# Optimization experiments

Measured on AMD Instinct MI355X. Metric: run time of the kernel, lower is better.

The kernel has to match this reference:

```python
import jax, jax.numpy as jnp
import numpy as np

NUM_HEADS = 8
NUM_KV_HEADS = 4
HEAD_DIM = 256
HIDDEN = 2048
SEQ = 4096
CHUNK_START = 2048
CHUNK_END = 4096
SOFTCAP = 50.0
EPS = 1e-6
ROPE_THETA = 10000.0
NEG_INF = -1e9


def _rms_norm(x, w, eps=EPS):
    # Gemma RMSNorm: computed in fp32, scale is (1 + w)
    x32 = x.astype(jnp.float32)
    out = x32 * jax.lax.rsqrt(jnp.mean(x32 * x32, axis=-1, keepdims=True) + eps)
    return (out * (1.0 + w.astype(jnp.float32))).astype(x.dtype)


def _rotate_half(x):
    h = x.shape[-1] // 2
    return jnp.concatenate([-x[..., h:], x[..., :h]], axis=-1)


def _apply_rope(x, cos, sin):
    # x: [B, S, H, D]; cos/sin: [B, S, D] -> unsqueeze head dim
    cos = cos[:, :, None, :]
    sin = sin[:, :, None, :]
    return x * cos + _rotate_half(x) * sin


def setup_inputs() -> dict:
    key = jax.random.key(0)
    ks = jax.random.split(key, 8)
    hidden_states = jax.random.normal(ks[0], (1, SEQ, HIDDEN), dtype=jnp.float32)
    # real RoPE tables
    inv_freq = 1.0 / (ROPE_THETA ** (np.arange(0, HEAD_DIM, 2, dtype=np.float32) / HEAD_DIM))
    pos = np.arange(SEQ, dtype=np.float32)
    freqs = np.outer(pos, inv_freq)                      # [S, D/2]
    emb = np.concatenate([freqs, freqs], axis=-1)        # [S, D]
    cos = jnp.asarray(np.cos(emb))[None]                 # [1, S, D]
    sin = jnp.asarray(np.sin(emb))[None]
    # causal additive mask for the chunk: query i (abs pos start+i) attends keys j <= start+i
    q_pos = np.arange(CHUNK_START, CHUNK_END)[:, None]
    k_pos = np.arange(CHUNK_END)[None, :]
    attention_mask = jnp.asarray(np.where(k_pos <= q_pos, 0.0, NEG_INF).astype(np.float32))[None, None]
    s = 0.02
    wq = jax.random.normal(ks[1], (HIDDEN, NUM_HEADS * HEAD_DIM), dtype=jnp.float32) * s
    wk = jax.random.normal(ks[2], (HIDDEN, NUM_KV_HEADS * HEAD_DIM), dtype=jnp.float32) * s
    wv = jax.random.normal(ks[3], (HIDDEN, NUM_KV_HEADS * HEAD_DIM), dtype=jnp.float32) * s
    wo = jax.random.normal(ks[4], (NUM_HEADS * HEAD_DIM, HIDDEN), dtype=jnp.float32) * s
    q_norm_w = jnp.zeros((HEAD_DIM,), dtype=jnp.float32)
    k_norm_w = jnp.zeros((HEAD_DIM,), dtype=jnp.float32)
    v_norm_w = jnp.zeros((HEAD_DIM,), dtype=jnp.float32)
    return {
        'hidden_states': hidden_states, 'cos': cos, 'sin': sin,
        'attention_mask': attention_mask,
        'wq': wq, 'wk': wk, 'wv': wv, 'wo': wo,
        'q_norm_w': q_norm_w, 'k_norm_w': k_norm_w, 'v_norm_w': v_norm_w,
        'start': CHUNK_START, 'end': CHUNK_END,
    }


def reference(hidden_states, cos, sin, attention_mask, wq, wk, wv, wo,
              q_norm_w, k_norm_w, v_norm_w, start, end):
    B = hidden_states.shape[0]
    chunk = end - start
    scaling = HEAD_DIM ** -0.5

    # ---- queries from the chunk ----
    q = (hidden_states[:, start:end] @ wq).reshape(B, chunk, NUM_HEADS, HEAD_DIM)
    q = _rms_norm(q, q_norm_w)
    q = _apply_rope(q, cos[:, start:end], sin[:, start:end])
    q = q.transpose(0, 2, 1, 3)                         # [B, H, chunk, D]

    # ---- keys / values over [0, end) ----
    kv_h = hidden_states[:, :end]
    k = (kv_h @ wk).reshape(B, end, NUM_KV_HEADS, HEAD_DIM)
    k = _rms_norm(k, k_norm_w)
    k = _apply_rope(k, cos[:, :end], sin[:, :end]).transpose(0, 2, 1, 3)   # [B, KV, end, D]
    v = (kv_h @ wv).reshape(B, end, NUM_KV_HEADS, HEAD_DIM)
    v = _rms_norm(v, v_norm_w).transpose(0, 2, 1, 3)                        # [B, KV, end, D]

    # ---- GQA repeat_kv ----
    n_rep = NUM_HEADS // NUM_KV_HEADS
    k = jnp.repeat(k, n_rep, axis=1)                    # [B, H, end, D]
    v = jnp.repeat(v, n_rep, axis=1)

    # ---- eager attention with logit softcap ----
    logits = jnp.einsum('bhqd,bhkd->bhqk', q, k) * scaling
    logits = jnp.tanh(logits / SOFTCAP) * SOFTCAP
    logits = logits + attention_mask
    attn = jax.nn.softmax(logits.astype(jnp.float32), axis=-1).astype(q.dtype)
    out = jnp.einsum('bhqk,bhkd->bhqd', attn, v)
    out = out.transpose(0, 2, 1, 3).reshape(B, chunk, NUM_HEADS * HEAD_DIM)
    return out @ wo
```

## Files before the change

kernel.cpp:

```cpp
#include <hip/hip_runtime.h>

#define HID 2048
#define SEQL 4096
#define CHUNK 2048
#define NHEADS 8
#define NKVH 4
#define HDIM 256

typedef __bf16 bf16x4 __attribute__((ext_vector_type(4)));
typedef __bf16 bf16x8 __attribute__((ext_vector_type(8)));
typedef float f32x4 __attribute__((ext_vector_type(4)));
typedef _Float16 f16x4 __attribute__((ext_vector_type(4)));
typedef __attribute__((address_space(1))) unsigned int* as1_u32;
typedef __attribute__((address_space(3))) unsigned int* as3_u32;

__device__ __forceinline__ void load_lds16(const __bf16* g, __bf16* l) {
  __builtin_amdgcn_global_load_lds((as1_u32)g, (as3_u32)l, 16, 0, 0);
}

__global__ void cvt_bf16_kernel(const float* __restrict__ X, __bf16* __restrict__ Y) {
  int i = blockIdx.x * blockDim.x + threadIdx.x;
  const float4* xv = (const float4*)X;
  float4 v = xv[i];
  bf16x4 o;
  o[0] = (__bf16)v.x; o[1] = (__bf16)v.y; o[2] = (__bf16)v.z; o[3] = (__bf16)v.w;
  *(bf16x4*)(Y + i * 4) = o;
}

__global__ void transpose_all_kernel(const float* __restrict__ wq, const float* __restrict__ wk,
                                     const float* __restrict__ wv, const float* __restrict__ wo,
                                     __bf16* __restrict__ WQT, __bf16* __restrict__ WKVT,
                                     __bf16* __restrict__ WOT) {
  __shared__ float tile[64][65];
  const int b = blockIdx.x;
  const float* W;
  __bf16* WT;
  int R, C, bx, by;
  if (b < 1024) { W = wq; WT = WQT; R = 2048; C = 2048; bx = b & 31; by = b >> 5; }
  else if (b < 1536) { int q = b - 1024; W = wk; WT = WKVT; R = 2048; C = 1024; bx = q & 15; by = q >> 4; }
  else if (b < 2048) { int q = b - 1536; W = wv; WT = WKVT + (size_t)1024 * 2048; R = 2048; C = 1024; bx = q & 15; by = q >> 4; }
  else { int q = b - 2048; W = wo; WT = WOT; R = 2048; C = 2048; bx = q & 31; by = q >> 5; }
  int r0 = by * 64, c0 = bx * 64;
  for (int i = threadIdx.x; i < 4096; i += 256) {
    int r = i >> 6, c = i & 63;
    tile[r][c] = W[(size_t)(r0 + r) * C + c0 + c];
  }
  __syncthreads();
  for (int i = threadIdx.x; i < 4096; i += 256) {
    int c = i >> 6, r = i & 63;
    WT[(size_t)(c0 + c) * R + r0 + r] = (__bf16)tile[r][c];
  }
}

template <int MODE>
__global__ __launch_bounds__(512, 2) void gemm256_kernel(
    const __bf16* __restrict__ A0, const __bf16* __restrict__ B0,
    const __bf16* __restrict__ B1, void* __restrict__ C0, void* __restrict__ C1) {
  __shared__ __bf16 Asm[2][256 * 64];
  __shared__ __bf16 Bsm[2][256 * 64];
  const int tid = threadIdx.x;
  const int lane = tid & 63, wave = tid >> 6;
  const int quad = lane >> 4, l15 = lane & 15;
  const int wm = (wave & 1) * 128, wn = (wave >> 1) * 64;

  const __bf16 *A, *B;
  char* Cb;
  int m0, n0;
  if (MODE == 0) {
    int b = blockIdx.x;
    if (b < 128) { A = A0; B = B0; Cb = (char*)C0; m0 = (b & 15) * 256; n0 = (b >> 4) * 256; }
    else { int q = b - 128; A = A0 + (size_t)2048 * 2048; B = B1; Cb = (char*)C1; m0 = (q & 7) * 256; n0 = (q >> 3) * 256; }
  } else {
    A = A0; B = B0; Cb = (char*)C0;
    m0 = (int)(blockIdx.x & 7) * 256; n0 = (int)(blockIdx.x >> 3) * 256;
  }

  f32x4 acc[8][4];
#pragma unroll
  for (int i = 0; i < 8; i++)
#pragma unroll
    for (int j = 0; j < 4; j++) acc[i][j] = (f32x4){0.f, 0.f, 0.f, 0.f};

  const int rr = tid >> 3;
  const int gch = (tid & 7) ^ ((tid >> 3) & 7);
  const int ldsb = wave * 512;

  const int sx = l15 & 7;
  const int s0 = ((0 + quad) ^ sx) * 8;
  const int s1 = ((4 + quad) ^ sx) * 8;

#define STAGE(T, BF)                                                                  \
  {                                                                                   \
    const int k0s = (T) * 64;                                                         \
    _Pragma("unroll")                                                                 \
    for (int a = 0; a < 4; a++) {                                                     \
      load_lds16(A + (size_t)(m0 + a * 64 + rr) * 2048 + k0s + gch * 8,               \
                 &Asm[BF][a * 4096 + ldsb]);                                          \
      load_lds16(B + (size_t)(n0 + a * 64 + rr) * 2048 + k0s + gch * 8,               \
                 &Bsm[BF][a * 4096 + ldsb]);                                          \
    }                                                                                 \
  }

#define LDA(MH, BF)                                                                   \
  _Pragma("unroll")                                                                   \
  for (int mi = 0; mi < 4; mi++) {                                                    \
    const int rowb = (wm + (MH) * 64 + mi * 16 + l15) * 64;                           \
    af[mi * 2 + 0] = *(const bf16x8*)(&Asm[BF][rowb + s0]);                           \
    af[mi * 2 + 1] = *(const bf16x8*)(&Asm[BF][rowb + s1]);                           \
  }

#define LDB(DST, NH, BF)                                                              \
  _Pragma("unroll")                                                                   \
  for (int ni = 0; ni < 2; ni++) {                                                    \
    const int rowb = (wn + (NH) * 32 + ni * 16 + l15) * 64;                           \
    DST[ni * 2 + 0] = *(const bf16x8*)(&Bsm[BF][rowb + s0]);                          \
    DST[ni * 2 + 1] = *(const bf16x8*)(&Bsm[BF][rowb + s1]);                          \
  }

#define MMA(MH, NH, BV)                                                               \
  __builtin_amdgcn_s_setprio(1);                                                      \
  _Pragma("unroll")                                                                   \
  for (int mi = 0; mi < 4; mi++)                                                      \
    _Pragma("unroll")                                                                 \
    for (int ni = 0; ni < 2; ni++) {                                                  \
      acc[(MH) * 4 + mi][(NH) * 2 + ni] = __builtin_amdgcn_mfma_f32_16x16x32_bf16(    \
          af[mi * 2 + 0], BV[ni * 2 + 0], acc[(MH) * 4 + mi][(NH) * 2 + ni], 0, 0, 0);\
      acc[(MH) * 4 + mi][(NH) * 2 + ni] = __builtin_amdgcn_mfma_f32_16x16x32_bf16(    \
          af[mi * 2 + 1], BV[ni * 2 + 1], acc[(MH) * 4 + mi][(NH) * 2 + ni], 0, 0, 0);\
    }                                                                                 \
  __builtin_amdgcn_s_setprio(0);

  bf16x8 af[8], bX[4], bY[4];

  STAGE(0, 0);
  STAGE(1, 1);
  asm volatile("s_waitcnt vmcnt(8)" ::: "memory");
  __builtin_amdgcn_s_barrier();

  const int NT = 32;
#pragma unroll 2
  for (int t = 0; t < NT; t++) {
    const int c = t & 1;
    LDA(0, c); LDB(bX, 0, c);
    __builtin_amdgcn_s_barrier();
    MMA(0, 0, bX);
    __builtin_amdgcn_s_barrier();
    LDB(bY, 1, c);
    __builtin_amdgcn_s_barrier();
    MMA(0, 1, bY);
    __builtin_amdgcn_s_barrier();
    LDA(1, c);
    __builtin_amdgcn_s_barrier();
    MMA(1, 1, bY);
    __builtin_amdgcn_s_barrier();
    LDB(bX, 0, c);
    __builtin_amdgcn_s_barrier();
    MMA(1, 0, bX);
    __builtin_amdgcn_s_barrier();
    if (t + 2 < NT) {
      STAGE(t + 2, c);
      asm volatile("s_waitcnt vmcnt(8)" ::: "memory");
      __builtin_amdgcn_s_barrier();
    } else if (t + 1 < NT) {
      asm volatile("s_waitcnt vmcnt(0)" ::: "memory");
      __builtin_amdgcn_s_barrier();
    }
  }

#pragma unroll
  for (int mh = 0; mh < 2; mh++)
#pragma unroll
    for (int mi = 0; mi < 4; mi++) {
      const int r = m0 + wm + mh * 64 + mi * 16 + quad * 4;
#pragma unroll
      for (int ni = 0; ni < 4; ni++) {
        const int cc = n0 + wn + (ni >> 1) * 32 + (ni & 1) * 16 + l15;
#pragma unroll
        for (int j = 0; j < 4; j++) {
          if (MODE == 1)
            ((float*)Cb)[(size_t)(r + j) * 2048 + cc] = acc[mh * 4 + mi][ni][j];
          else
            ((__bf16*)Cb)[(size_t)(r + j) * 2048 + cc] = (__bf16)acc[mh * 4 + mi][ni][j];
        }
      }
    }
#undef STAGE
#undef LDA
#undef LDB
#undef MMA
}

template <int NI, bool F32OUT>
__global__ __launch_bounds__(256, 2) void gemm_bt_kernel(
    const __bf16* __restrict__ A, const __bf16* __restrict__ B,
    void* __restrict__ Cv, int M, int N, int Kd) {
  constexpr int BN = NI * 32;
  __shared__ __bf16 Asm[2][128 * 32];
  __shared__ __bf16 Bsm[2][BN * 32];
  const int tid = threadIdx.x;
  const int lane = tid & 63, wave = tid >> 6;
  const int quad = lane >> 4, l15 = lane & 15;
  const int m0 = blockIdx.x * 128, n0 = blockIdx.y * BN;
  const int wm = (wave & 1) * 64, wn = (wave >> 1) * (NI * 16);
  f32x4 acc[4][NI];
#pragma unroll
  for (int i = 0; i < 4; i++)
#pragma unroll
    for (int j = 0; j < NI; j++) acc[i][j] = (f32x4){0.f, 0.f, 0.f, 0.f};

  const int rA = lane >> 2, cA = (lane & 3) * 8;

#pragma unroll
  for (int c = wave; c < 8; c += 4)
    load_lds16(A + (size_t)(m0 + c * 16 + rA) * Kd + cA, &Asm[0][c * 512]);
#pragma unroll
  for (int c = wave; c < BN / 16; c += 4)
    load_lds16(B + (size_t)(n0 + c * 16 + rA) * Kd + cA, &Bsm[0][c * 512]);

  for (int k0 = 0; k0 < Kd; k0 += 32) {
    const int buf = (k0 >> 5) & 1;
    __syncthreads();
    if (k0 + 32 < Kd) {
#pragma unroll
      for (int c = wave; c < 8; c += 4)
        load_lds16(A + (size_t)(m0 + c * 16 + rA) * Kd + k0 + 32 + cA, &Asm[buf ^ 1][c * 512]);
#pragma unroll
      for (int c = wave; c < BN / 16; c += 4)
        load_lds16(B + (size_t)(n0 + c * 16 + rA) * Kd + k0 + 32 + cA, &Bsm[buf ^ 1][c * 512]);
    }
    bf16x8 af[4], bfr[NI];
#pragma unroll
    for (int i = 0; i < 4; i++)
      af[i] = *(const bf16x8*)(&Asm[buf][(wm + i * 16 + l15) * 32 + quad * 8]);
#pragma unroll
    for (int i = 0; i < NI; i++)
      bfr[i] = *(const bf16x8*)(&Bsm[buf][(wn + i * 16 + l15) * 32 + quad * 8]);
#pragma unroll
    for (int mi = 0; mi < 4; mi++)
#pragma unroll
      for (int ni = 0; ni < NI; ni++)
        acc[mi][ni] = __builtin_amdgcn_mfma_f32_16x16x32_bf16(af[mi], bfr[ni], acc[mi][ni], 0, 0, 0);
  }
#pragma unroll
  for (int mi = 0; mi < 4; mi++) {
    int r = m0 + wm + mi * 16 + quad * 4;
#pragma unroll
    for (int ni = 0; ni < NI; ni++) {
      int cc = n0 + wn + ni * 16 + l15;
#pragma unroll
      for (int j = 0; j < 4; j++) {
        if (F32OUT)
          ((float*)Cv)[(size_t)(r + j) * N + cc] = acc[mi][ni][j];
        else
          ((__bf16*)Cv)[(size_t)(r + j) * N + cc] = (__bf16)acc[mi][ni][j];
      }
    }
  }
}

__global__ void norm_all_kernel(__bf16* __restrict__ Qp, __bf16* __restrict__ KVp,
                                const float* __restrict__ cosb, const float* __restrict__ sinb,
                                const float* __restrict__ qw, const float* __restrict__ kw,
                                const float* __restrict__ vw) {
  const int gw = (blockIdx.x * 256 + threadIdx.x) >> 6;
  const int lane = threadIdx.x & 63;
  const int d0 = lane * 4;

  __bf16* row;
  const float* w;
  int pos = -1;
  bool isV = false;
  float prescale = 1.f;
  if (gw < 16384) {
    int t = gw >> 3, h = gw & 7;
    row = Qp + (size_t)t * 2048 + h * 256;
    w = qw; pos = t + 2048; prescale = 0.0625f;
  } else {
    int g2 = gw - 16384;
    int t = g2 >> 3, r = g2 & 7;
    if (r < 4) {
      row = KVp + (size_t)t * 2048 + r * 256;
      w = kw; pos = t;
    } else {
      row = KVp + (size_t)t * 2048 + 1024 + (r - 4) * 256;
      w = vw; isV = true;
    }
  }

  bf16x4 rv = *(const bf16x4*)(row + d0);
  float x[4];
  float ss = 0.f;
#pragma unroll
  for (int j = 0; j < 4; j++) { x[j] = (float)rv[j]; ss += x[j] * x[j]; }
#pragma unroll
  for (int off = 1; off < 64; off <<= 1) ss += __shfl_xor(ss, off);
  float scale = rsqrtf(ss * (1.f / 256.f) + 1e-6f);
  float n[4];
#pragma unroll
  for (int j = 0; j < 4; j++) n[j] = x[j] * scale * (1.f + w[d0 + j]);

  if (!isV) {
    const float* cp = cosb + (size_t)pos * 256 + d0;
    const float* sp = sinb + (size_t)pos * 256 + d0;
    bf16x4 ov;
#pragma unroll
    for (int j = 0; j < 4; j++) {
      float other = __shfl_xor(n[j], 32);
      float rot = (lane < 32) ? -other : other;
      ov[j] = (__bf16)((n[j] * cp[j] + rot * sp[j]) * prescale);
    }
    *(bf16x4*)(row + d0) = ov;
  } else {
    bf16x4 ov;
#pragma unroll
    for (int j = 0; j < 4; j++) ov[j] = (__bf16)n[j];
    *(bf16x4*)(row + d0) = ov;
  }
}

__global__ void vtrans_kernel(const __bf16* __restrict__ KVp, __bf16* __restrict__ VT) {
  __shared__ __bf16 tile[64][72];
  const int b = blockIdx.x;
  const int h = b >> 8;
  const int r = b & 255;
  const int t0 = (r >> 2) * 64;
  const int d0 = (r & 3) * 64;
  const __bf16* src = KVp + 1024 + h * 256 + d0;
#pragma unroll
  for (int it = 0; it < 2; it++) {
    int idx = it * 256 + threadIdx.x;
    int tt = idx >> 3, dd = (idx & 7) * 8;
    *(bf16x8*)(&tile[tt][dd]) = *(const bf16x8*)(src + (size_t)(t0 + tt) * 2048 + dd);
  }
  __syncthreads();
  __bf16* dst = VT + (size_t)h * (256 * 4096) + (size_t)d0 * 4096 + t0;
#pragma unroll
  for (int it = 0; it < 2; it++) {
    int idx = it * 256 + threadIdx.x;
    int dd = idx >> 3, tt = (idx & 7) * 8;
    bf16x8 o;
#pragma unroll
    for (int j = 0; j < 8; j++) o[j] = tile[tt + j][dd];
    *(bf16x8*)(dst + (size_t)dd * 4096 + tt) = o;
  }
}

__global__ __launch_bounds__(256, 2) void attn_kernel(
    const __bf16* __restrict__ Q,
    const __bf16* __restrict__ K,
    const __bf16* __restrict__ VT,
    _Float16* __restrict__ Op,
    float* __restrict__ Lp) {
  __shared__ __bf16 Ksm[2][8][32][32];
  __shared__ __bf16 Vsm[2][256][32];
  __shared__ __bf16 Pex[4][32][40];
  const int tid = threadIdx.x;
  const int lane = tid & 63, wave = tid >> 6;
  const int quad = lane >> 4, l15 = lane & 15;
  const int b = blockIdx.x;
  const int idx = b & 255;
  const int h = idx & 7, sp = (idx >> 3) & 3;
  int qt = idx >> 5;
  if (b >= 256) qt = 15 - qt;
  const int kvh = h >> 1;

  const int T = 68 + 4 * qt;
  const int nst = T >> 2;

  bf16x8 qf[2][8];
#pragma unroll
  for (int r = 0; r < 2; r++) {
    const __bf16* qp = Q + (size_t)(qt * 128 + wave * 32 + r * 16 + l15) * 2048 + h * 256 + quad * 8;
#pragma unroll
    for (int s = 0; s < 8; s++) qf[r][s] = *(const bf16x8*)(qp + s * 32);
  }
  f32x4 o[2][16];
#pragma unroll
  for (int r = 0; r < 2; r++)
#pragma unroll
    for (int i = 0; i < 16; i++) o[r][i] = (f32x4){0.f, 0.f, 0.f, 0.f};
  float rs[2][4] = {{0.f, 0.f, 0.f, 0.f}, {0.f, 0.f, 0.f, 0.f}};

  const __bf16* Kb = K + kvh * 256;
  const __bf16* Vb = VT + (size_t)kvh * (256 * 4096);
  const int rA = lane >> 2;
  const int cAs = (((lane & 3) ^ ((rA >> 1) & 3)) * 8);
  const int kx = (quad ^ ((l15 >> 1) & 3)) * 8;
  const int qbase = 2048 + qt * 128 + wave * 32 + quad * 4;

  {
    const int t0 = sp * 32;
#pragma unroll
    for (int ch = 0; ch < 4; ch++) {
      int cc = wave + ch * 4;
      int s = cc >> 1, hf = cc & 1;
      load_lds16(Kb + (size_t)(t0 + hf * 16 + rA) * 2048 + s * 32 + cAs, &Ksm[0][s][hf * 16][0]);
      load_lds16(Vb + (size_t)(cc * 16 + rA) * 4096 + t0 + cAs, &Vsm[0][cc * 16][0]);
    }
  }

  for (int i = 0; i < nst; i++) {
    const int buf = i & 1;
    const int t0 = (4 * i + sp) * 32;
    __syncthreads();
    if (i + 1 < nst) {
      const int t1 = t0 + 128;
#pragma unroll
      for (int ch = 0; ch < 4; ch++) {
        int cc = wave + ch * 4;
        int s = cc >> 1, hf = cc & 1;
        load_lds16(Kb + (size_t)(t1 + hf * 16 + rA) * 2048 + s * 32 + cAs, &Ksm[buf ^ 1][s][hf * 16][0]);
        load_lds16(Vb + (size_t)(cc * 16 + rA) * 4096 + t1 + cAs, &Vsm[buf ^ 1][cc * 16][0]);
      }
    }

    f32x4 s4[2][2];
    s4[0][0] = (f32x4){0.f, 0.f, 0.f, 0.f};
    s4[0][1] = s4[0][0]; s4[1][0] = s4[0][0]; s4[1][1] = s4[0][0];
#pragma unroll
    for (int s = 0; s < 8; s++) {
      bf16x8 b0 = *(const bf16x8*)(&Ksm[buf][s][l15][kx]);
      bf16x8 b1 = *(const bf16x8*)(&Ksm[buf][s][16 + l15][kx]);
      s4[0][0] = __builtin_amdgcn_mfma_f32_16x16x32_bf16(qf[0][s], b0, s4[0][0], 0, 0, 0);
      s4[0][1] = __builtin_amdgcn_mfma_f32_16x16x32_bf16(qf[0][s], b1, s4[0][1], 0, 0, 0);
      s4[1][0] = __builtin_amdgcn_mfma_f32_16x16x32_bf16(qf[1][s], b0, s4[1][0], 0, 0, 0);
      s4[1][1] = __builtin_amdgcn_mfma_f32_16x16x32_bf16(qf[1][s], b1, s4[1][1], 0, 0, 0);
    }

    const bool mk = (i == nst - 1);
#pragma unroll
    for (int r = 0; r < 2; r++)
#pragma unroll
      for (int nt = 0; nt < 2; nt++) {
        const int key = t0 + nt * 16 + l15;
#pragma unroll
        for (int j = 0; j < 4; j++) {
          float v = s4[r][nt][j];
          float e = __expf(v * 0.04f);
          float p = __expf(-100.f * __builtin_amdgcn_rcpf(e + 1.f));
          if (mk && key > qbase + r * 16 + j) p = 0.f;
          s4[r][nt][j] = p;
          rs[r][j] += p;
        }
      }

#pragma unroll
    for (int r = 0; r < 2; r++)
#pragma unroll
      for (int nt = 0; nt < 2; nt++)
#pragma unroll
        for (int j = 0; j < 4; j++)
          Pex[wave][r * 16 + quad * 4 + j][nt * 16 + l15] = (__bf16)s4[r][nt][j];

    bf16x8 pf0 = *(const bf16x8*)(&Pex[wave][l15][quad * 8]);
    bf16x8 pf1 = *(const bf16x8*)(&Pex[wave][16 + l15][quad * 8]);
#pragma unroll
    for (int d = 0; d < 16; d++) {
      bf16x8 vf = *(const bf16x8*)(&Vsm[buf][d * 16 + l15][kx]);
      o[0][d] = __builtin_amdgcn_mfma_f32_16x16x32_bf16(pf0, vf, o[0][d], 0, 0, 0);
      o[1][d] = __builtin_amdgcn_mfma_f32_16x16x32_bf16(pf1, vf, o[1][d], 0, 0, 0);
    }
  }

#pragma unroll
  for (int off = 1; off < 16; off <<= 1)
#pragma unroll
    for (int r = 0; r < 2; r++)
#pragma unroll
      for (int j = 0; j < 4; j++) rs[r][j] += __shfl_xor(rs[r][j], off);

  _Float16* Os = Op + (size_t)sp * (2048 * 2048);
  float* Ls = Lp + sp * (2048 * 8);
#pragma unroll
  for (int r = 0; r < 2; r++) {
    float inv[4];
#pragma unroll
    for (int j = 0; j < 4; j++)
      inv[j] = rs[r][j] > 0.f ? 1.f / rs[r][j] : 0.f;
    const int trow = qt * 128 + wave * 32 + r * 16 + quad * 4;
#pragma unroll
    for (int d = 0; d < 16; d++) {
      const int col = h * 256 + d * 16 + l15;
#pragma unroll
      for (int j = 0; j < 4; j++)
        Os[(size_t)(trow + j) * 2048 + col] = (_Float16)(o[r][d][j] * inv[j]);
    }
    if (l15 == 0) {
#pragma unroll
      for (int j = 0; j < 4; j++) Ls[(trow + j) * 8 + h] = rs[r][j];
    }
  }
}

__global__ void merge_kernel(const _Float16* __restrict__ Op, const float* __restrict__ Lp,
                             __bf16* __restrict__ AO) {
  int f = (blockIdx.x * 256 + threadIdx.x) * 4;
  int q = f >> 11, col = f & 2047, h = col >> 8;
  float lsum = 0.f;
  float acc[4] = {0.f, 0.f, 0.f, 0.f};
#pragma unroll
  for (int s = 0; s < 4; s++) {
    float l = Lp[s * (2048 * 8) + q * 8 + h];
    lsum += l;
    f16x4 v = *(const f16x4*)(Op + (size_t)s * (2048 * 2048) + f);
#pragma unroll
    for (int j = 0; j < 4; j++) acc[j] += l * (float)v[j];
  }
  float inv = 1.f / lsum;
  bf16x4 o;
#pragma unroll
  for (int j = 0; j < 4; j++) o[j] = (__bf16)(acc[j] * inv);
  *(bf16x4*)(AO + f) = o;
}

extern "C" void kernel_launch(void* const* d_in, const int* in_sizes, int n_in,
                              void* d_out, int out_size, void* d_ws, size_t ws_size,
                              hipStream_t stream) {
  const float* hidden = (const float*)d_in[0];
  const float* cosb = (const float*)d_in[1];
  const float* sinb = (const float*)d_in[2];
  const float* wq = (const float*)d_in[4];
  const float* wk = (const float*)d_in[5];
  const float* wv = (const float*)d_in[6];
  const float* wo = (const float*)d_in[7];
  const float* qw = (const float*)d_in[8];
  const float* kw = (const float*)d_in[9];
  const float* vw = (const float*)d_in[10];
  float* outp = (float*)d_out;

  char* p = (char*)d_ws;
  __bf16* Xb = (__bf16*)p;   p += (size_t)SEQL * HID * 2;
  __bf16* WQT = (__bf16*)p;  p += (size_t)2048 * 2048 * 2;
  __bf16* WKVT = (__bf16*)p; p += (size_t)2048 * 2048 * 2;
  __bf16* WOT = (__bf16*)p;  p += (size_t)2048 * 2048 * 2;
  __bf16* Qp = (__bf16*)p;   p += (size_t)2048 * 2048 * 2;
  __bf16* KVp = (__bf16*)p;  p += (size_t)4096 * 2048 * 2;
  __bf16* VT = (__bf16*)p;   p += (size_t)4 * 256 * 4096 * 2;
  __bf16* AO = (__bf16*)p;   p += (size_t)2048 * 2048 * 2;
  float* Lpart = (float*)p;  p += (size_t)4 * 2048 * 8 * 4;
  _Float16* Opart = (_Float16*)Xb;

  cvt_bf16_kernel<<<8192, 256, 0, stream>>>(hidden, Xb);
  transpose_all_kernel<<<3072, 256, 0, stream>>>(wq, wk, wv, wo, WQT, WKVT, WOT);

  gemm256_kernel<0><<<192, 512, 0, stream>>>(Xb, WKVT, WQT, KVp, Qp);

  norm_all_kernel<<<12288, 256, 0, stream>>>(Qp, KVp, cosb, sinb, qw, kw, vw);
  vtrans_kernel<<<1024, 256, 0, stream>>>(KVp, VT);

  attn_kernel<<<512, 256, 0, stream>>>(Qp, KVp, VT, Opart, Lpart);
  merge_kernel<<<4096, 256, 0, stream>>>(Opart, Lpart, AO);

  gemm_bt_kernel<2, true><<<dim3(16, 32), 256, 0, stream>>>(AO, WOT, outp, 2048, 2048, 2048);
}
```

Measured before the change: 379.6 us.

## Vectorize weight transpose, drop intra-tile barriers in QKV GEMM, retile output GEMM

The weight transpose kernel now reads float4 and writes packed bf16x8 vectors instead of scalar accesses, cutting memory transactions. The main 256x256 GEMM loop drops the per-phase workgroup barriers and setprio hints, loads both B halves up front and keeps bX live, so it no longer reloads it. The output projection GEMM switches its template tile parameter from 2 to 4 and halves the grid's y dimension. Removing barriers gives the compiler more scheduling freedom but raises register pressure and gives up the wave-phase coordination those barriers provided.

Measured after the change: 366.7 us. 3.4% less time.

```diff
diff --git a/kernel.cpp b/kernel.cpp
--- a/kernel.cpp
+++ b/kernel.cpp
@@ -41,14 +41,22 @@
   else if (b < 2048) { int q = b - 1536; W = wv; WT = WKVT + (size_t)1024 * 2048; R = 2048; C = 1024; bx = q & 15; by = q >> 4; }
   else { int q = b - 2048; W = wo; WT = WOT; R = 2048; C = 2048; bx = q & 31; by = q >> 5; }
   int r0 = by * 64, c0 = bx * 64;
-  for (int i = threadIdx.x; i < 4096; i += 256) {
-    int r = i >> 6, c = i & 63;
-    tile[r][c] = W[(size_t)(r0 + r) * C + c0 + c];
+#pragma unroll
+  for (int it = 0; it < 4; it++) {
+    int idx = it * 256 + threadIdx.x;
+    int r = idx >> 4, c4 = (idx & 15) * 4;
+    float4 v = *(const float4*)&W[(size_t)(r0 + r) * C + c0 + c4];
+    tile[r][c4] = v.x; tile[r][c4 + 1] = v.y; tile[r][c4 + 2] = v.z; tile[r][c4 + 3] = v.w;
   }
   __syncthreads();
-  for (int i = threadIdx.x; i < 4096; i += 256) {
-    int c = i >> 6, r = i & 63;
-    WT[(size_t)(c0 + c) * R + r0 + r] = (__bf16)tile[r][c];
+#pragma unroll
+  for (int it = 0; it < 2; it++) {
+    int idx = it * 256 + threadIdx.x;
+    int cc = idx >> 3, rb = (idx & 7) * 8;
+    bf16x8 o;
+#pragma unroll
+    for (int j = 0; j < 8; j++) o[j] = (__bf16)tile[rb + j][cc];
+    *(bf16x8*)&WT[(size_t)(c0 + cc) * R + r0 + rb] = o;
   }
 }
 
@@ -118,7 +126,6 @@
   }
 
 #define MMA(MH, NH, BV)                                                               \
-  __builtin_amdgcn_s_setprio(1);                                                      \
   _Pragma("unroll")                                                                   \
   for (int mi = 0; mi < 4; mi++)                                                      \
     _Pragma("unroll")                                                                 \
@@ -127,8 +134,7 @@
           af[mi * 2 + 0], BV[ni * 2 + 0], acc[(MH) * 4 + mi][(NH) * 2 + ni], 0, 0, 0);\
       acc[(MH) * 4 + mi][(NH) * 2 + ni] = __builtin_amdgcn_mfma_f32_16x16x32_bf16(    \
           af[mi * 2 + 1], BV[ni * 2 + 1], acc[(MH) * 4 + mi][(NH) * 2 + ni], 0, 0, 0);\
-    }                                                                                 \
-  __builtin_amdgcn_s_setprio(0);
+    }
 
   bf16x8 af[8], bX[4], bY[4];
 
@@ -141,20 +147,13 @@
 #pragma unroll 2
   for (int t = 0; t < NT; t++) {
     const int c = t & 1;
-    LDA(0, c); LDB(bX, 0, c);
-    __builtin_amdgcn_s_barrier();
+    LDA(0, c);
+    LDB(bX, 0, c);
+    LDB(bY, 1, c);
     MMA(0, 0, bX);
-    __builtin_amdgcn_s_barrier();
-    LDB(bY, 1, c);
-    __builtin_amdgcn_s_barrier();
     MMA(0, 1, bY);
-    __builtin_amdgcn_s_barrier();
     LDA(1, c);
-    __builtin_amdgcn_s_barrier();
     MMA(1, 1, bY);
-    __builtin_amdgcn_s_barrier();
-    LDB(bX, 0, c);
-    __builtin_amdgcn_s_barrier();
     MMA(1, 0, bX);
     __builtin_amdgcn_s_barrier();
     if (t + 2 < NT) {
@@ -551,5 +550,5 @@
   attn_kernel<<<512, 256, 0, stream>>>(Qp, KVp, VT, Opart, Lpart);
   merge_kernel<<<4096, 256, 0, stream>>>(Opart, Lpart, AO);
 
-  gemm_bt_kernel<2, true><<<dim3(16, 32), 256, 0, stream>>>(AO, WOT, outp, 2048, 2048, 2048);
-}
+  gemm_bt_kernel<4, true><<<dim3(16, 16), 256, 0, stream>>>(AO, WOT, outp, 2048, 2048, 2048);
+}
```
